# Optimization experiments

Measured on AMD Instinct MI355X. Metric: run time of the kernel, lower is better.

The kernel has to match this reference:

```python
import jax, jax.numpy as jnp
import numpy as np

T = 25
H1, H2, H3 = 16, 72, 32


def _lin_params(key, out_dim, in_dim):
    k1, k2 = jax.random.split(key)
    s = 1.0 / np.sqrt(in_dim)
    W = jax.random.uniform(k1, (out_dim, in_dim), jnp.float32, -s, s)
    b = jax.random.uniform(k2, (out_dim,), jnp.float32, -s, s)
    return W, b


def _lstm_params(key, in_dim, hid):
    k1, k2, k3, k4 = jax.random.split(key, 4)
    s = 1.0 / np.sqrt(hid)
    Wih = jax.random.uniform(k1, (4 * hid, in_dim), jnp.float32, -s, s)
    Whh = jax.random.uniform(k2, (4 * hid, hid), jnp.float32, -s, s)
    bih = jax.random.uniform(k3, (4 * hid,), jnp.float32, -s, s)
    bhh = jax.random.uniform(k4, (4 * hid,), jnp.float32, -s, s)
    return Wih, Whh, bih, bhh


def setup_inputs() -> dict:
    key = jax.random.key(0)
    ks = jax.random.split(key, 9)
    B = 131072
    x = jax.random.normal(ks[0], (B, T, 2), jnp.float32)
    y = jax.random.normal(ks[1], (B, T, 36), jnp.float32)
    Wih1, Whh1, bih1, bhh1 = _lstm_params(ks[2], 2, H1)
    Wih2, Whh2, bih2, bhh2 = _lstm_params(ks[3], H2, H2)
    Wih3, Whh3, bih3, bhh3 = _lstm_params(ks[4], H1 + H2, H3)
    W1, b1 = _lin_params(ks[5], 64, 36)
    W2, b2 = _lin_params(ks[6], H2, 64)
    W3, b3 = _lin_params(ks[7], 16, H3)
    W4, b4 = _lin_params(ks[8], 2, 16)
    return dict(x=x, y=y,
                Wih1=Wih1, Whh1=Whh1, bih1=bih1, bhh1=bhh1,
                Wih2=Wih2, Whh2=Whh2, bih2=bih2, bhh2=bhh2,
                Wih3=Wih3, Whh3=Whh3, bih3=bih3, bhh3=bhh3,
                W1=W1, b1=b1, W2=W2, b2=b2, W3=W3, b3=b3, W4=W4, b4=b4)


def _lstm_cell(xt, h, c, Wih, Whh, bih, bhh):
    # PyTorch LSTMCell gate order: i, f, g, o
    g = xt @ Wih.T + bih + h @ Whh.T + bhh
    i, f, gg, o = jnp.split(g, 4, axis=-1)
    c_new = jax.nn.sigmoid(f) * c + jax.nn.sigmoid(i) * jnp.tanh(gg)
    h_new = jax.nn.sigmoid(o) * jnp.tanh(c_new)
    return h_new, c_new


def _forward(x, y, Wih1, Whh1, bih1, bhh1, Wih2, Whh2, bih2, bhh2,
             Wih3, Whh3, bih3, bhh3, W1, b1, W2, b2, W3, b3, W4, b4):
    B = x.shape[0]
    init = (jnp.zeros((B, H1), jnp.float32), jnp.zeros((B, H1), jnp.float32),
            jnp.zeros((B, H2), jnp.float32), jnp.zeros((B, H2), jnp.float32),
            jnp.zeros((B, H3), jnp.float32), jnp.zeros((B, H3), jnp.float32))

    def step(carry, inp):
        h1, c1, h2, c2, h3, c3 = carry
        xt, yt = inp  # [B,2], [B,36]
        h1, c1 = _lstm_cell(xt, h1, c1, Wih1, Whh1, bih1, bhh1)
        l2 = jax.nn.relu(yt @ W1.T + b1) @ W2.T + b2
        h2, c2 = _lstm_cell(l2, h2, c2, Wih2, Whh2, bih2, bhh2)
        h = jnp.concatenate([h1, h2], axis=1)
        h3, c3 = _lstm_cell(h, h3, c3, Wih3, Whh3, bih3, bhh3)
        out = jax.nn.relu(h3 @ W3.T + b3) @ W4.T + b4  # [B,2]
        return (h1, c1, h2, c2, h3, c3), out

    xs = (jnp.swapaxes(x, 0, 1), jnp.swapaxes(y, 0, 1))  # [T,B,*]
    _, outs = jax.lax.scan(step, init, xs)  # [T,B,2]
    # torch.cat(outputs, dim=1) -> [B, T*2]
    return jnp.swapaxes(outs, 0, 1).reshape(B, T * 2)


def reference(x, y, Wih1, Whh1, bih1, bhh1, Wih2, Whh2, bih2, bhh2,
              Wih3, Whh3, bih3, bhh3, W1, b1, W2, b2, W3, b3, W4, b4):
    return _forward(x, y, Wih1, Whh1, bih1, bhh1, Wih2, Whh2, bih2, bhh2,
                    Wih3, Whh3, bih3, bhh3, W1, b1, W2, b2, W3, b3, W4, b4)
```

## Files before the change

### kernel.cpp

```cpp
#include <hip/hip_runtime.h>
#include <hip/hip_bf16.h>

#define THREADS 1024

typedef __hip_bfloat16 bf16;
typedef __attribute__((ext_vector_type(4))) float f32x4;
typedef __attribute__((ext_vector_type(16))) float f32x16;
typedef __attribute__((ext_vector_type(8))) short bf16x8;

#define MFMA32 __builtin_amdgcn_mfma_f32_32x32x16_bf16
#define Z16 f32x16{0.f,0.f,0.f,0.f,0.f,0.f,0.f,0.f,0.f,0.f,0.f,0.f,0.f,0.f,0.f,0.f}

#define O_A1  0
#define O_AY  4096
#define O_AT1 10240
#define O_A2  20480
#define O_AH3 40960
#define LDS_ELEMS 45056
#define LDS_BYTES (LDS_ELEMS * 2)

__device__ __forceinline__ int blk(int KC, int nt, int kc, int slot) {
    return ((nt * KC + kc) * 2 + slot) << 9;
}
__device__ __forceinline__ int eix(int col, int kl) {
    return ((col | ((kl >> 3) << 5)) << 3) + (kl & 7);
}

__device__ __forceinline__ float rcp_(float x) { return __builtin_amdgcn_rcpf(x); }

__device__ __forceinline__ float lstm_ew1(f32x4 acc, float& cst) {
    float ei = __expf(-acc[0]);
    float ef = __expf(-acc[1]);
    float eg = __expf(2.0f * fminf(acc[2], 40.0f));
    float eo = __expf(-acc[3]);
    float c = rcp_(1.0f + ef) * cst + (eg - 1.0f) * rcp_((1.0f + ei) * (eg + 1.0f));
    cst = c;
    float ec = __expf(2.0f * fminf(c, 40.0f));
    return (ec - 1.0f) * rcp_((1.0f + eo) * (ec + 1.0f));
}

__device__ __forceinline__ ushort bfu(float f) {
    union { bf16 b; ushort u; } v; v.b = __float2bfloat16(f); return v.u;
}

template <typename F>
__device__ __forceinline__ bf16x8 mk32(int lane, F val) {
    union { bf16x8 v; bf16 h[8]; } u;
#pragma unroll
    for (int j = 0; j < 8; ++j)
        u.h[j] = __float2bfloat16(val(((lane >> 5) << 3) + j));
    return u.v;
}

__global__ void __launch_bounds__(THREADS, 4)
lstm_fused(const float* __restrict__ x, const float* __restrict__ y,
           const float* __restrict__ Wih1, const float* __restrict__ Whh1,
           const float* __restrict__ bih1, const float* __restrict__ bhh1,
           const float* __restrict__ Wih2, const float* __restrict__ Whh2,
           const float* __restrict__ bih2, const float* __restrict__ bhh2,
           const float* __restrict__ Wih3, const float* __restrict__ Whh3,
           const float* __restrict__ bih3, const float* __restrict__ bhh3,
           const float* __restrict__ W1, const float* __restrict__ b1,
           const float* __restrict__ W2, const float* __restrict__ b2,
           const float* __restrict__ W3, const float* __restrict__ b3,
           const float* __restrict__ W4, const float* __restrict__ b4,
           float* __restrict__ out) {
    extern __shared__ char smem[];
    bf16* sb = (bf16*)smem;
    const int tid = threadIdx.x;
    const int wave = tid >> 6, lane = tid & 63;
    const int ln31 = lane & 31, hi = lane >> 5;
    const int b0 = blockIdx.x * 64;

    bf16x8 W[11];
#pragma unroll
    for (int i = 0; i < 11; ++i) W[i] = bf16x8{0, 0, 0, 0, 0, 0, 0, 0};

    if (wave < 9) {
        int n = 32 * wave + ln31;
        int r = (n & 3) * 72 + (n >> 2);
        float bias = bih2[r] + bhh2[r];
#pragma unroll
        for (int kc = 0; kc < 10; ++kc)
            W[kc] = mk32(lane, [&](int k) {
                int kg = kc * 16 + k;
                return kg < 72 ? Wih2[r * 72 + kg]
                     : (kg < 144 ? Whh2[r * 72 + (kg - 72)]
                     : (kg == 144 ? bias : 0.0f)); });
    } else if (wave < 13) {
        int n = 32 * (wave - 9) + ln31;
        int r = (n & 3) * 32 + (n >> 2);
        float bias = bih3[r] + bhh3[r];
        W[0] = mk32(lane, [&](int k) {
            return k < 2 ? 0.0f : Wih3[r * 88 + (k - 2)]; });
        W[1] = mk32(lane, [&](int k) {
            int kg = 16 + k;
            return kg < 18 ? Wih3[r * 88 + (kg - 2)] : (kg == 18 ? bias : 0.0f); });
#pragma unroll
        for (int i = 0; i < 5; ++i)
            W[2 + i] = mk32(lane, [&](int k) {
                int kg = 64 + i * 16 + k;
                return kg < 72 ? 0.0f : Wih3[r * 88 + 16 + (kg - 72)]; });
#pragma unroll
        for (int i = 0; i < 2; ++i)
            W[7 + i] = mk32(lane, [&](int k) { return Whh3[r * 32 + i * 16 + k]; });
        if (wave < 11) {
#pragma unroll
            for (int i = 0; i < 2; ++i)
                W[9 + i] = mk32(lane, [&](int k) {
                    return (ln31 < 16) ? W3[ln31 * 32 + i * 16 + k] : 0.0f; });
        }
    } else {
        if (wave < 15) {
            int n = 32 * (wave - 13) + ln31;
            int r = (n & 3) * 16 + (n >> 2);
            float bias = bih1[r] + bhh1[r];
            W[0] = mk32(lane, [&](int k) {
                return k < 2 ? Wih1[r * 2 + k] : Whh1[r * 16 + (k - 2)]; });
            W[1] = mk32(lane, [&](int k) {
                int kg = 16 + k;
                return kg < 18 ? Whh1[r * 16 + (kg - 2)] : (kg == 18 ? bias : 0.0f); });
        }
        {
            int n2 = 32 * (wave - 13) + ln31;
#pragma unroll
            for (int kc = 0; kc < 5; ++kc)
                W[2 + kc] = mk32(lane, [&](int k) {
                    int kg = kc * 16 + k;
                    if (n2 >= 72) return 0.0f;
                    return kg < 64 ? W2[n2 * 64 + kg] : (kg == 64 ? b2[n2] : 0.0f); });
        }
        if (wave >= 14) {
            int f = 32 * (wave - 14) + ln31;
#pragma unroll
            for (int kc = 0; kc < 3; ++kc)
                W[7 + kc] = mk32(lane, [&](int k) {
                    int kg = kc * 16 + k;
                    return kg < 36 ? W1[f * 36 + kg] : (kg == 36 ? b1[f] : 0.0f); });
        }
    }

    {
        int4* z = (int4*)sb;
        int4 zv = {0, 0, 0, 0};
        for (int i = tid; i < LDS_BYTES / 16; i += THREADS) z[i] = zv;
    }
    __syncthreads();
    for (int it = tid; it < 2 * 2304; it += THREADS) {
        int slot = it / 2304, r2 = it - slot * 2304;
        int m = r2 / 36, k = r2 - m * 36;
        sb[O_AY + blk(3, m >> 5, k >> 4, slot) + eix(m & 31, k & 15)] =
            __float2bfloat16(y[(size_t)(b0 + m) * 900 + slot * 36 + k]);
    }
    if (tid < 128) {
        int m = tid >> 1, k = tid & 1;
        sb[O_A1 + blk(2, m >> 5, 0, 0) + eix(m & 31, k)] =
            __float2bfloat16(x[(size_t)(b0 + m) * 50 + k]);
    }
    {
        const bf16 one = __float2bfloat16(1.0f);
        int i = tid & 127, col = i & 31, nt = (i >> 5) & 1, s = (i >> 6) & 1;
        if (tid < 128)       sb[O_A1 + blk(2, nt, 1, s) + eix(col, 2)] = one;
        else if (tid < 256)  sb[O_AY + blk(3, nt, 2, s) + eix(col, 4)] = one;
        else if (tid < 384)  sb[O_AT1 + blk(5, nt, 4, s) + eix(col, 0)] = one;
        else if (tid < 512)  sb[O_A2 + blk(10, nt, 9, s) + eix(col, 0)] = one;
    }
    __syncthreads();
    if (wave >= 14) {
#pragma unroll
        for (int s = 0; s < 2; ++s) {
#pragma unroll
            for (int nt = 0; nt < 2; ++nt) {
                f32x16 acc = Z16;
#pragma unroll
                for (int kc = 0; kc < 3; ++kc) {
                    bf16x8 a = *(const bf16x8*)(sb + O_AY + blk(3, nt, kc, s) + (lane << 3));
                    acc = MFMA32(W[7 + kc], a, acc, 0, 0, 0);
                }
#pragma unroll
                for (int qq = 0; qq < 4; ++qq) {
                    int f0 = 32 * (wave - 14) + 8 * qq + 4 * hi;
                    ushort4 pk;
                    pk.x = bfu(fmaxf(acc[4 * qq + 0], 0.f));
                    pk.y = bfu(fmaxf(acc[4 * qq + 1], 0.f));
                    pk.z = bfu(fmaxf(acc[4 * qq + 2], 0.f));
                    pk.w = bfu(fmaxf(acc[4 * qq + 3], 0.f));
                    *(ushort4*)(sb + O_AT1 + blk(5, nt, f0 >> 4, s ^ 1) + eix(ln31, f0 & 15)) = pk;
                }
            }
        }
    }
    __syncthreads();
    if (wave >= 13) {
#pragma unroll
        for (int nt = 0; nt < 2; ++nt) {
            f32x16 acc = Z16;
#pragma unroll
            for (int kc = 0; kc < 5; ++kc) {
                bf16x8 a = *(const bf16x8*)(sb + O_AT1 + blk(5, nt, kc, 1) + (lane << 3));
                acc = MFMA32(W[2 + kc], a, acc, 0, 0, 0);
            }
#pragma unroll
            for (int qq = 0; qq < 4; ++qq) {
                int n0 = 32 * (wave - 13) + 8 * qq + 4 * hi;
                if (n0 < 72) {
                    ushort4 pk;
                    pk.x = bfu(acc[4 * qq + 0]); pk.y = bfu(acc[4 * qq + 1]);
                    pk.z = bfu(acc[4 * qq + 2]); pk.w = bfu(acc[4 * qq + 3]);
                    *(ushort4*)(sb + O_A2 + blk(10, nt, n0 >> 4, 0) + eix(ln31, n0 & 15)) = pk;
                }
            }
        }
    } else if (wave == 11 || wave == 12) {
        const int half = wave - 11;
        const int m = 32 * half + (lane >> 1);
        const float* yp = y + (size_t)(b0 + m) * 900 + 2 * 36;
#pragma unroll
        for (int c = (lane & 1); c < 9; c += 2) {
            float4 v = *(const float4*)(yp + 4 * c);
            ushort4 pk;
            pk.x = bfu(v.x); pk.y = bfu(v.y); pk.z = bfu(v.z); pk.w = bfu(v.w);
            int k0 = 4 * c;
            *(ushort4*)(sb + O_AY + blk(3, half, k0 >> 4, 0) + eix(m & 31, k0 & 15)) = pk;
        }
    }
    float cS[2][4] = {};
    __syncthreads();

    for (int t = 0; t <= 25; ++t) {
        const int p = t & 1, q = p ^ 1;

        if (wave < 9) {
            if (t <= 24) {
#pragma unroll
                for (int nt = 0; nt < 2; ++nt) {
                    f32x16 acc = Z16;
#pragma unroll
                    for (int kc = 0; kc < 10; ++kc) {
                        bf16x8 a = *(const bf16x8*)(sb + O_A2 + blk(10, nt, kc, p) + (lane << 3));
                        acc = MFMA32(W[kc], a, acc, 0, 0, 0);
                    }
#pragma unroll
                    for (int qq = 0; qq < 4; ++qq) {
                        f32x4 g4 = {acc[4 * qq], acc[4 * qq + 1], acc[4 * qq + 2], acc[4 * qq + 3]};
                        float hv = lstm_ew1(g4, cS[nt][qq]);
                        int k = 72 + 8 * wave + 2 * qq + hi;
                        sb[O_A2 + blk(10, nt, k >> 4, q) + eix(ln31, k & 15)] = __float2bfloat16(hv);
                    }
                }
            }
        } else if (wave < 13) {
            if (t >= 1) {
                const int M3 = wave - 9;
#pragma unroll
                for (int nt = 0; nt < 2; ++nt) {
                    f32x16 acc = Z16;
                    {
                        bf16x8 a0 = *(const bf16x8*)(sb + O_A1 + blk(2, nt, 0, p) + (lane << 3));
                        acc = MFMA32(W[0], a0, acc, 0, 0, 0);
                        bf16x8 a1 = *(const bf16x8*)(sb + O_A1 + blk(2, nt, 1, p) + (lane << 3));
                        acc = MFMA32(W[1], a1, acc, 0, 0, 0);
                    }
#pragma unroll
                    for (int i = 0; i < 5; ++i) {
                        bf16x8 a = *(const bf16x8*)(sb + O_A2 + blk(10, nt, 4 + i, p) + (lane << 3));
                        acc = MFMA32(W[2 + i], a, acc, 0, 0, 0);
                    }
#pragma unroll
                    for (int i = 0; i < 2; ++i) {
                        bf16x8 a = *(const bf16x8*)(sb + O_AH3 + blk(2, nt, i, p) + (lane << 3));
                        acc = MFMA32(W[7 + i], a, acc, 0, 0, 0);
                    }
#pragma unroll
                    for (int qq = 0; qq < 4; ++qq) {
                        f32x4 g4 = {acc[4 * qq], acc[4 * qq + 1], acc[4 * qq + 2], acc[4 * qq + 3]};
                        float hv = lstm_ew1(g4, cS[nt][qq]);
                        int k = 8 * M3 + 2 * qq + hi;
                        sb[O_AH3 + blk(2, nt, k >> 4, q) + eix(ln31, k & 15)] = __float2bfloat16(hv);
                    }
                }
            }
            if (wave < 11) {
                if (t >= 2) {
                    const int ntw = wave - 9;
                    f32x16 acc = Z16;
#pragma unroll
                    for (int i = 0; i < 2; ++i) {
                        bf16x8 a = *(const bf16x8*)(sb + O_AH3 + blk(2, ntw, i, p) + (lane << 3));
                        acc = MFMA32(W[9 + i], a, acc, 0, 0, 0);
                    }
                    float s0 = 0.f, s1 = 0.f;
#pragma unroll
                    for (int qq = 0; qq < 2; ++qq) {
                        int r = 8 * qq + 4 * hi;
                        float4 b3v = *(const float4*)(b3 + r);
                        float4 w0v = *(const float4*)(W4 + r);
                        float4 w1v = *(const float4*)(W4 + 16 + r);
#pragma unroll
                        for (int s = 0; s < 4; ++s) {
                            float u = fmaxf(acc[4 * qq + s] + b3v[s], 0.f);
                            s0 = fmaf(u, w0v[s], s0);
                            s1 = fmaf(u, w1v[s], s1);
                        }
                    }
                    s0 += __shfl_xor(s0, 32); s1 += __shfl_xor(s1, 32);
                    if (lane < 32) {
                        float2 o; o.x = s0 + b4[0]; o.y = s1 + b4[1];
                        *(float2*)(out + (size_t)(b0 + 32 * ntw + ln31) * 50 + (t - 2) * 2) = o;
                    }
                }
            } else if (t <= 21) {
                const int half = wave - 11;
                const int m = 32 * half + (lane >> 1);
                const float* yp = y + (size_t)(b0 + m) * 900 + (t + 3) * 36;
#pragma unroll
                for (int c = (lane & 1); c < 9; c += 2) {
                    float4 v = *(const float4*)(yp + 4 * c);
                    ushort4 pk;
                    pk.x = bfu(v.x); pk.y = bfu(v.y); pk.z = bfu(v.z); pk.w = bfu(v.w);
                    int k0 = 4 * c;
                    *(ushort4*)(sb + O_AY + blk(3, half, k0 >> 4, q) + eix(m & 31, k0 & 15)) = pk;
                }
            }
        } else {
            if (t <= 24 && wave < 15) {
                const int M1 = wave - 13;
#pragma unroll
                for (int nt = 0; nt < 2; ++nt) {
                    f32x16 acc = Z16;
#pragma unroll
                    for (int i = 0; i < 2; ++i) {
                        bf16x8 a = *(const bf16x8*)(sb + O_A1 + blk(2, nt, i, p) + (lane << 3));
                        acc = MFMA32(W[i], a, acc, 0, 0, 0);
                    }
#pragma unroll
                    for (int qq = 0; qq < 4; ++qq) {
                        f32x4 g4 = {acc[4 * qq], acc[4 * qq + 1], acc[4 * qq + 2], acc[4 * qq + 3]};
                        float hv = lstm_ew1(g4, cS[nt][qq]);
                        int k = 2 + 8 * M1 + 2 * qq + hi;
                        sb[O_A1 + blk(2, nt, k >> 4, q) + eix(ln31, k & 15)] = __float2bfloat16(hv);
                    }
                }
            }
            if (t <= 23 && wave == 13) {
                const int nt = lane >> 5;
                float2 xv = *(const float2*)(x + (size_t)(b0 + lane) * 50 + (t + 1) * 2);
                union { uint u; ushort s[2]; } xu;
                xu.s[0] = bfu(xv.x); xu.s[1] = bfu(xv.y);
                *(uint*)(sb + O_A1 + blk(2, nt, 0, q) + (ln31 << 3)) = xu.u;
            }
            if (t <= 22 && wave >= 14) {
#pragma unroll
                for (int nt = 0; nt < 2; ++nt) {
                    f32x16 acc = Z16;
#pragma unroll
                    for (int kc = 0; kc < 3; ++kc) {
                        bf16x8 a = *(const bf16x8*)(sb + O_AY + blk(3, nt, kc, p) + (lane << 3));
                        acc = MFMA32(W[7 + kc], a, acc, 0, 0, 0);
                    }
#pragma unroll
                    for (int qq = 0; qq < 4; ++qq) {
                        int f0 = 32 * (wave - 14) + 8 * qq + 4 * hi;
                        ushort4 pk;
                        pk.x = bfu(fmaxf(acc[4 * qq + 0], 0.f));
                        pk.y = bfu(fmaxf(acc[4 * qq + 1], 0.f));
                        pk.z = bfu(fmaxf(acc[4 * qq + 2], 0.f));
                        pk.w = bfu(fmaxf(acc[4 * qq + 3], 0.f));
                        *(ushort4*)(sb + O_AT1 + blk(5, nt, f0 >> 4, q) + eix(ln31, f0 & 15)) = pk;
                    }
                }
            }
            if (t <= 23) {
#pragma unroll
                for (int nt = 0; nt < 2; ++nt) {
                    f32x16 acc = Z16;
#pragma unroll
                    for (int kc = 0; kc < 5; ++kc) {
                        bf16x8 a = *(const bf16x8*)(sb + O_AT1 + blk(5, nt, kc, p) + (lane << 3));
                        acc = MFMA32(W[2 + kc], a, acc, 0, 0, 0);
                    }
#pragma unroll
                    for (int qq = 0; qq < 4; ++qq) {
                        int n0 = 32 * (wave - 13) + 8 * qq + 4 * hi;
                        if (n0 < 72) {
                            ushort4 pk;
                            pk.x = bfu(acc[4 * qq + 0]); pk.y = bfu(acc[4 * qq + 1]);
                            pk.z = bfu(acc[4 * qq + 2]); pk.w = bfu(acc[4 * qq + 3]);
                            *(ushort4*)(sb + O_A2 + blk(10, nt, n0 >> 4, q) + eix(ln31, n0 & 15)) = pk;
                        }
                    }
                }
            }
        }
        __syncthreads();
    }

    if (wave == 9 || wave == 10) {
        const int ntw = wave - 9;
        f32x16 acc = Z16;
#pragma unroll
        for (int i = 0; i < 2; ++i) {
            bf16x8 a = *(const bf16x8*)(sb + O_AH3 + blk(2, ntw, i, 0) + (lane << 3));
            acc = MFMA32(W[9 + i], a, acc, 0, 0, 0);
        }
        float s0 = 0.f, s1 = 0.f;
#pragma unroll
        for (int qq = 0; qq < 2; ++qq) {
            int r = 8 * qq + 4 * hi;
            float4 b3v = *(const float4*)(b3 + r);
            float4 w0v = *(const float4*)(W4 + r);
            float4 w1v = *(const float4*)(W4 + 16 + r);
#pragma unroll
            for (int s = 0; s < 4; ++s) {
                float u = fmaxf(acc[4 * qq + s] + b3v[s], 0.f);
                s0 = fmaf(u, w0v[s], s0);
                s1 = fmaf(u, w1v[s], s1);
            }
        }
        s0 += __shfl_xor(s0, 32); s1 += __shfl_xor(s1, 32);
        if (lane < 32) {
            float2 o; o.x = s0 + b4[0]; o.y = s1 + b4[1];
            *(float2*)(out + (size_t)(b0 + 32 * ntw + ln31) * 50 + 24 * 2) = o;
        }
    }
}

extern "C" void kernel_launch(void* const* d_in, const int* in_sizes, int n_in,
                              void* d_out, int out_size, void* d_ws, size_t ws_size,
                              hipStream_t stream) {
    (void)in_sizes; (void)n_in; (void)d_ws; (void)ws_size; (void)out_size;
    hipFuncSetAttribute((const void*)lstm_fused,
                        hipFuncAttributeMaxDynamicSharedMemorySize, LDS_BYTES);
    lstm_fused<<<dim3(2048), dim3(THREADS), LDS_BYTES, stream>>>(
        (const float*)d_in[0], (const float*)d_in[1],
        (const float*)d_in[2], (const float*)d_in[3],
        (const float*)d_in[4], (const float*)d_in[5],
        (const float*)d_in[6], (const float*)d_in[7],
        (const float*)d_in[8], (const float*)d_in[9],
        (const float*)d_in[10], (const float*)d_in[11],
        (const float*)d_in[12], (const float*)d_in[13],
        (const float*)d_in[14], (const float*)d_in[15],
        (const float*)d_in[16], (const float*)d_in[17],
        (const float*)d_in[18], (const float*)d_in[19],
        (const float*)d_in[20], (const float*)d_in[21],
        (float*)d_out);
}
```

Before: 944.3 us.

## Fold exp2 scaling into LSTM weights and restructure per-step load/compute/store scheduling

Pre-scales gate weights and biases by -log2(e), or by 2*log2(e) for the g gate, so the gate nonlinearities use raw exp2 without a multiply. Restructures each timestep so all LDS operand loads for both tiles are issued up front and the MFMAs run back to back, with the elementwise work and LDS stores deferred to the end. Global loads for y and x are issued early to overlap latency. The output head now reuses the h3 operands already in registers instead of re-reading them from LDS. This raises register pressure, which could hurt occupancy or cause spills.

```diff
diff --git a/kernel.cpp b/kernel.cpp
--- a/kernel.cpp
+++ b/kernel.cpp
@@ -27,15 +27,22 @@
 }
 
 __device__ __forceinline__ float rcp_(float x) { return __builtin_amdgcn_rcpf(x); }
-
-__device__ __forceinline__ float lstm_ew1(f32x4 acc, float& cst) {
-    float ei = __expf(-acc[0]);
-    float ef = __expf(-acc[1]);
-    float eg = __expf(2.0f * fminf(acc[2], 40.0f));
-    float eo = __expf(-acc[3]);
+__device__ __forceinline__ float exp2_(float x) {
+#if __has_builtin(__builtin_amdgcn_exp2f)
+    return __builtin_amdgcn_exp2f(x);
+#else
+    return exp2f(x);
+#endif
+}
+
+__device__ __forceinline__ float lstm_ew1(f32x4 a, float& cst) {
+    float ei = exp2_(a[0]);
+    float ef = exp2_(a[1]);
+    float eg = exp2_(fminf(a[2], 115.0f));
+    float eo = exp2_(a[3]);
     float c = rcp_(1.0f + ef) * cst + (eg - 1.0f) * rcp_((1.0f + ei) * (eg + 1.0f));
     cst = c;
-    float ec = __expf(2.0f * fminf(c, 40.0f));
+    float ec = exp2_(fminf(c * 2.885390082f, 115.0f));
     return (ec - 1.0f) * rcp_((1.0f + eo) * (ec + 1.0f));
 }
 
@@ -80,30 +87,33 @@
         int n = 32 * wave + ln31;
         int r = (n & 3) * 72 + (n >> 2);
         float bias = bih2[r] + bhh2[r];
+        float sc = ((n & 3) == 2) ? 2.885390082f : -1.442695041f;
 #pragma unroll
         for (int kc = 0; kc < 10; ++kc)
             W[kc] = mk32(lane, [&](int k) {
                 int kg = kc * 16 + k;
-                return kg < 72 ? Wih2[r * 72 + kg]
-                     : (kg < 144 ? Whh2[r * 72 + (kg - 72)]
-                     : (kg == 144 ? bias : 0.0f)); });
+                float v = kg < 72 ? Wih2[r * 72 + kg]
+                       : (kg < 144 ? Whh2[r * 72 + (kg - 72)]
+                       : (kg == 144 ? bias : 0.0f));
+                return sc * v; });
     } else if (wave < 13) {
         int n = 32 * (wave - 9) + ln31;
         int r = (n & 3) * 32 + (n >> 2);
         float bias = bih3[r] + bhh3[r];
+        float sc = ((n & 3) == 2) ? 2.885390082f : -1.442695041f;
         W[0] = mk32(lane, [&](int k) {
-            return k < 2 ? 0.0f : Wih3[r * 88 + (k - 2)]; });
+            return sc * (k < 2 ? 0.0f : Wih3[r * 88 + (k - 2)]); });
         W[1] = mk32(lane, [&](int k) {
             int kg = 16 + k;
-            return kg < 18 ? Wih3[r * 88 + (kg - 2)] : (kg == 18 ? bias : 0.0f); });
+            return sc * (kg < 18 ? Wih3[r * 88 + (kg - 2)] : (kg == 18 ? bias : 0.0f)); });
 #pragma unroll
         for (int i = 0; i < 5; ++i)
             W[2 + i] = mk32(lane, [&](int k) {
                 int kg = 64 + i * 16 + k;
-                return kg < 72 ? 0.0f : Wih3[r * 88 + 16 + (kg - 72)]; });
+                return sc * (kg < 72 ? 0.0f : Wih3[r * 88 + 16 + (kg - 72)]); });
 #pragma unroll
         for (int i = 0; i < 2; ++i)
-            W[7 + i] = mk32(lane, [&](int k) { return Whh3[r * 32 + i * 16 + k]; });
+            W[7 + i] = mk32(lane, [&](int k) { return sc * Whh3[r * 32 + i * 16 + k]; });
         if (wave < 11) {
 #pragma unroll
             for (int i = 0; i < 2; ++i)
@@ -115,11 +125,12 @@
             int n = 32 * (wave - 13) + ln31;
             int r = (n & 3) * 16 + (n >> 2);
             float bias = bih1[r] + bhh1[r];
+            float sc = ((n & 3) == 2) ? 2.885390082f : -1.442695041f;
             W[0] = mk32(lane, [&](int k) {
-                return k < 2 ? Wih1[r * 2 + k] : Whh1[r * 16 + (k - 2)]; });
+                return sc * (k < 2 ? Wih1[r * 2 + k] : Whh1[r * 16 + (k - 2)]); });
             W[1] = mk32(lane, [&](int k) {
                 int kg = 16 + k;
-                return kg < 18 ? Whh1[r * 16 + (kg - 2)] : (kg == 18 ? bias : 0.0f); });
+                return sc * (kg < 18 ? Whh1[r * 16 + (kg - 2)] : (kg == 18 ? bias : 0.0f)); });
         }
         {
             int n2 = 32 * (wave - 13) + ln31;
@@ -232,164 +243,239 @@
 
         if (wave < 9) {
             if (t <= 24) {
-#pragma unroll
-                for (int nt = 0; nt < 2; ++nt) {
-                    f32x16 acc = Z16;
-#pragma unroll
-                    for (int kc = 0; kc < 10; ++kc) {
-                        bf16x8 a = *(const bf16x8*)(sb + O_A2 + blk(10, nt, kc, p) + (lane << 3));
-                        acc = MFMA32(W[kc], a, acc, 0, 0, 0);
+                bf16x8 al[10], bl[10];
+#pragma unroll
+                for (int kc = 0; kc < 10; ++kc)
+                    al[kc] = *(const bf16x8*)(sb + O_A2 + blk(10, 0, kc, p) + (lane << 3));
+                f32x16 acc0 = Z16;
+#pragma unroll
+                for (int kc = 0; kc < 10; ++kc) acc0 = MFMA32(W[kc], al[kc], acc0, 0, 0, 0);
+#pragma unroll
+                for (int kc = 0; kc < 10; ++kc)
+                    bl[kc] = *(const bf16x8*)(sb + O_A2 + blk(10, 1, kc, p) + (lane << 3));
+                f32x16 acc1 = Z16;
+#pragma unroll
+                for (int kc = 0; kc < 10; ++kc) acc1 = MFMA32(W[kc], bl[kc], acc1, 0, 0, 0);
+                ushort hv0[4], hv1[4];
+#pragma unroll
+                for (int qq = 0; qq < 4; ++qq) {
+                    f32x4 g4 = {acc0[4 * qq], acc0[4 * qq + 1], acc0[4 * qq + 2], acc0[4 * qq + 3]};
+                    hv0[qq] = bfu(lstm_ew1(g4, cS[0][qq]));
+                }
+#pragma unroll
+                for (int qq = 0; qq < 4; ++qq) {
+                    f32x4 g4 = {acc1[4 * qq], acc1[4 * qq + 1], acc1[4 * qq + 2], acc1[4 * qq + 3]};
+                    hv1[qq] = bfu(lstm_ew1(g4, cS[1][qq]));
+                }
+#pragma unroll
+                for (int qq = 0; qq < 4; ++qq) {
+                    int k = 72 + 8 * wave + 2 * qq + hi;
+                    *(ushort*)(sb + O_A2 + blk(10, 0, k >> 4, q) + eix(ln31, k & 15)) = hv0[qq];
+                    *(ushort*)(sb + O_A2 + blk(10, 1, k >> 4, q) + eix(ln31, k & 15)) = hv1[qq];
+                }
+            }
+        } else if (wave < 13) {
+            const bool ystage = (wave >= 11) && (t <= 21);
+            float4 yv[5];
+            if (ystage) {
+                const int m = 32 * (wave - 11) + (lane >> 1);
+                const float* yp = y + (size_t)(b0 + m) * 900 + (t + 3) * 36;
+#pragma unroll
+                for (int i = 0; i < 5; ++i) {
+                    int c = 2 * i + (lane & 1);
+                    if (c < 9) yv[i] = *(const float4*)(yp + 4 * c);
+                }
+            }
+            ushort hv0[4], hv1[4];
+            bf16x8 ahw0 = {}, ahw1 = {};
+            if (t >= 1) {
+                bf16x8 a[9], b[9];
+                a[0] = *(const bf16x8*)(sb + O_A1 + blk(2, 0, 0, p) + (lane << 3));
+                a[1] = *(const bf16x8*)(sb + O_A1 + blk(2, 0, 1, p) + (lane << 3));
+#pragma unroll
+                for (int i = 0; i < 5; ++i)
+                    a[2 + i] = *(const bf16x8*)(sb + O_A2 + blk(10, 0, 4 + i, p) + (lane << 3));
+                a[7] = *(const bf16x8*)(sb + O_AH3 + blk(2, 0, 0, p) + (lane << 3));
+                a[8] = *(const bf16x8*)(sb + O_AH3 + blk(2, 0, 1, p) + (lane << 3));
+                f32x16 acc0 = Z16;
+#pragma unroll
+                for (int i = 0; i < 9; ++i) acc0 = MFMA32(W[i], a[i], acc0, 0, 0, 0);
+                b[0] = *(const bf16x8*)(sb + O_A1 + blk(2, 1, 0, p) + (lane << 3));
+                b[1] = *(const bf16x8*)(sb + O_A1 + blk(2, 1, 1, p) + (lane << 3));
+#pragma unroll
+                for (int i = 0; i < 5; ++i)
+                    b[2 + i] = *(const bf16x8*)(sb + O_A2 + blk(10, 1, 4 + i, p) + (lane << 3));
+                b[7] = *(const bf16x8*)(sb + O_AH3 + blk(2, 1, 0, p) + (lane << 3));
+                b[8] = *(const bf16x8*)(sb + O_AH3 + blk(2, 1, 1, p) + (lane << 3));
+                f32x16 acc1 = Z16;
+#pragma unroll
+                for (int i = 0; i < 9; ++i) acc1 = MFMA32(W[i], b[i], acc1, 0, 0, 0);
+                if (wave == 9)  { ahw0 = a[7]; ahw1 = a[8]; }
+                if (wave == 10) { ahw0 = b[7]; ahw1 = b[8]; }
+#pragma unroll
+                for (int qq = 0; qq < 4; ++qq) {
+                    f32x4 g4 = {acc0[4 * qq], acc0[4 * qq + 1], acc0[4 * qq + 2], acc0[4 * qq + 3]};
+                    hv0[qq] = bfu(lstm_ew1(g4, cS[0][qq]));
+                }
+#pragma unroll
+                for (int qq = 0; qq < 4; ++qq) {
+                    f32x4 g4 = {acc1[4 * qq], acc1[4 * qq + 1], acc1[4 * qq + 2], acc1[4 * qq + 3]};
+                    hv1[qq] = bfu(lstm_ew1(g4, cS[1][qq]));
+                }
+            }
+            if (t >= 2 && wave < 11) {
+                const int ntw = wave - 9;
+                f32x16 acc = Z16;
+                acc = MFMA32(W[9], ahw0, acc, 0, 0, 0);
+                acc = MFMA32(W[10], ahw1, acc, 0, 0, 0);
+                float s0 = 0.f, s1 = 0.f;
+#pragma unroll
+                for (int qq = 0; qq < 2; ++qq) {
+                    int r = 8 * qq + 4 * hi;
+                    float4 b3v = *(const float4*)(b3 + r);
+                    float4 w0v = *(const float4*)(W4 + r);
+                    float4 w1v = *(const float4*)(W4 + 16 + r);
+#pragma unroll
+                    for (int s = 0; s < 4; ++s) {
+                        float u = fmaxf(acc[4 * qq + s] + b3v[s], 0.f);
+                        s0 = fmaf(u, w0v[s], s0);
+                        s1 = fmaf(u, w1v[s], s1);
                     }
-#pragma unroll
-                    for (int qq = 0; qq < 4; ++qq) {
-                        f32x4 g4 = {acc[4 * qq], acc[4 * qq + 1], acc[4 * qq + 2], acc[4 * qq + 3]};
-                        float hv = lstm_ew1(g4, cS[nt][qq]);
-                        int k = 72 + 8 * wave + 2 * qq + hi;
-                        sb[O_A2 + blk(10, nt, k >> 4, q) + eix(ln31, k & 15)] = __float2bfloat16(hv);
-                    }
-                }
-            }
-        } else if (wave < 13) {
+                }
+                s0 += __shfl_xor(s0, 32); s1 += __shfl_xor(s1, 32);
+                if (lane < 32) {
+                    float2 o; o.x = s0 + b4[0]; o.y = s1 + b4[1];
+                    *(float2*)(out + (size_t)(b0 + 32 * ntw + ln31) * 50 + (t - 2) * 2) = o;
+                }
+            }
             if (t >= 1) {
                 const int M3 = wave - 9;
 #pragma unroll
+                for (int qq = 0; qq < 4; ++qq) {
+                    int k = 8 * M3 + 2 * qq + hi;
+                    *(ushort*)(sb + O_AH3 + blk(2, 0, k >> 4, q) + eix(ln31, k & 15)) = hv0[qq];
+                    *(ushort*)(sb + O_AH3 + blk(2, 1, k >> 4, q) + eix(ln31, k & 15)) = hv1[qq];
+                }
+            }
+            if (ystage) {
+                const int m = 32 * (wave - 11) + (lane >> 1);
+#pragma unroll
+                for (int i = 0; i < 5; ++i) {
+                    int c = 2 * i + (lane & 1);
+                    if (c < 9) {
+                        ushort4 pk;
+                        pk.x = bfu(yv[i].x); pk.y = bfu(yv[i].y);
+                        pk.z = bfu(yv[i].z); pk.w = bfu(yv[i].w);
+                        int k0 = 4 * c;
+                        *(ushort4*)(sb + O_AY + blk(3, wave - 11, k0 >> 4, q) + eix(m & 31, k0 & 15)) = pk;
+                    }
+                }
+            }
+        } else {
+            float2 xv = {0.f, 0.f};
+            if (wave == 13 && t <= 23)
+                xv = *(const float2*)(x + (size_t)(b0 + lane) * 50 + (t + 1) * 2);
+            ushort hva[4], hvb[4];
+            if (t <= 24 && wave < 15) {
+                bf16x8 a0 = *(const bf16x8*)(sb + O_A1 + blk(2, 0, 0, p) + (lane << 3));
+                bf16x8 a1 = *(const bf16x8*)(sb + O_A1 + blk(2, 0, 1, p) + (lane << 3));
+                bf16x8 c0 = *(const bf16x8*)(sb + O_A1 + blk(2, 1, 0, p) + (lane << 3));
+                bf16x8 c1 = *(const bf16x8*)(sb + O_A1 + blk(2, 1, 1, p) + (lane << 3));
+                f32x16 acc0 = Z16, acc1 = Z16;
+                acc0 = MFMA32(W[0], a0, acc0, 0, 0, 0);
+                acc0 = MFMA32(W[1], a1, acc0, 0, 0, 0);
+                acc1 = MFMA32(W[0], c0, acc1, 0, 0, 0);
+                acc1 = MFMA32(W[1], c1, acc1, 0, 0, 0);
+#pragma unroll
+                for (int qq = 0; qq < 4; ++qq) {
+                    f32x4 g4 = {acc0[4 * qq], acc0[4 * qq + 1], acc0[4 * qq + 2], acc0[4 * qq + 3]};
+                    hva[qq] = bfu(lstm_ew1(g4, cS[0][qq]));
+                }
+#pragma unroll
+                for (int qq = 0; qq < 4; ++qq) {
+                    f32x4 g4 = {acc1[4 * qq], acc1[4 * qq + 1], acc1[4 * qq + 2], acc1[4 * qq + 3]};
+                    hvb[qq] = bfu(lstm_ew1(g4, cS[1][qq]));
+                }
+            }
+            ushort4 f1p[2][4];
+            if (t <= 22 && wave >= 14) {
+#pragma unroll
                 for (int nt = 0; nt < 2; ++nt) {
+                    bf16x8 a0 = *(const bf16x8*)(sb + O_AY + blk(3, nt, 0, p) + (lane << 3));
+                    bf16x8 a1 = *(const bf16x8*)(sb + O_AY + blk(3, nt, 1, p) + (lane << 3));
+                    bf16x8 a2 = *(const bf16x8*)(sb + O_AY + blk(3, nt, 2, p) + (lane << 3));
                     f32x16 acc = Z16;
-                    {
-                        bf16x8 a0 = *(const bf16x8*)(sb + O_A1 + blk(2, nt, 0, p) + (lane << 3));
-                        acc = MFMA32(W[0], a0, acc, 0, 0, 0);
-                        bf16x8 a1 = *(const bf16x8*)(sb + O_A1 + blk(2, nt, 1, p) + (lane << 3));
-                        acc = MFMA32(W[1], a1, acc, 0, 0, 0);
-                    }
-#pragma unroll
-                    for (int i = 0; i < 5; ++i) {
-                        bf16x8 a = *(const bf16x8*)(sb + O_A2 + blk(10, nt, 4 + i, p) + (lane << 3));
-                        acc = MFMA32(W[2 + i], a, acc, 0, 0, 0);
-                    }
-#pragma unroll
-                    for (int i = 0; i < 2; ++i) {
-                        bf16x8 a = *(const bf16x8*)(sb + O_AH3 + blk(2, nt, i, p) + (lane << 3));
-                        acc = MFMA32(W[7 + i], a, acc, 0, 0, 0);
-                    }
+                    acc = MFMA32(W[7], a0, acc, 0, 0, 0);
+                    acc = MFMA32(W[8], a1, acc, 0, 0, 0);
+                    acc = MFMA32(W[9], a2, acc, 0, 0, 0);
 #pragma unroll
                     for (int qq = 0; qq < 4; ++qq) {
-                        f32x4 g4 = {acc[4 * qq], acc[4 * qq + 1], acc[4 * qq + 2], acc[4 * qq + 3]};
-                        float hv = lstm_ew1(g4, cS[nt][qq]);
-                        int k = 8 * M3 + 2 * qq + hi;
-                        sb[O_AH3 + blk(2, nt, k >> 4, q) + eix(ln31, k & 15)] = __float2bfloat16(hv);
-                    }
-                }
-            }
-            if (wave < 11) {
-                if (t >= 2) {
-                    const int ntw = wave - 9;
-                    f32x16 acc = Z16;
-#pragma unroll
-                    for (int i = 0; i < 2; ++i) {
-                        bf16x8 a = *(const bf16x8*)(sb + O_AH3 + blk(2, ntw, i, p) + (lane << 3));
-                        acc = MFMA32(W[9 + i], a, acc, 0, 0, 0);
-                    }
-                    float s0 = 0.f, s1 = 0.f;
-#pragma unroll
-                    for (int qq = 0; qq < 2; ++qq) {
-                        int r = 8 * qq + 4 * hi;
-                        float4 b3v = *(const float4*)(b3 + r);
-                        float4 w0v = *(const float4*)(W4 + r);
-                        float4 w1v = *(const float4*)(W4 + 16 + r);
-#pragma unroll
-                        for (int s = 0; s < 4; ++s) {
-                            float u = fmaxf(acc[4 * qq + s] + b3v[s], 0.f);
-                            s0 = fmaf(u, w0v[s], s0);
-                            s1 = fmaf(u, w1v[s], s1);
-                        }
-                    }
-                    s0 += __shfl_xor(s0, 32); s1 += __shfl_xor(s1, 32);
-                    if (lane < 32) {
-                        float2 o; o.x = s0 + b4[0]; o.y = s1 + b4[1];
-                        *(float2*)(out + (size_t)(b0 + 32 * ntw + ln31) * 50 + (t - 2) * 2) = o;
-                    }
-                }
-            } else if (t <= 21) {
-                const int half = wave - 11;
-                const int m = 32 * half + (lane >> 1);
-                const float* yp = y + (size_t)(b0 + m) * 900 + (t + 3) * 36;
-#pragma unroll
-                for (int c = (lane & 1); c < 9; c += 2) {
-                    float4 v = *(const float4*)(yp + 4 * c);
-                    ushort4 pk;
-                    pk.x = bfu(v.x); pk.y = bfu(v.y); pk.z = bfu(v.z); pk.w = bfu(v.w);
-                    int k0 = 4 * c;
-                    *(ushort4*)(sb + O_AY + blk(3, half, k0 >> 4, q) + eix(m & 31, k0 & 15)) = pk;
-                }
-            }
-        } else {
-            if (t <= 24 && wave < 15) {
-                const int M1 = wave - 13;
-#pragma unroll
-                for (int nt = 0; nt < 2; ++nt) {
-                    f32x16 acc = Z16;
-#pragma unroll
-                    for (int i = 0; i < 2; ++i) {
-                        bf16x8 a = *(const bf16x8*)(sb + O_A1 + blk(2, nt, i, p) + (lane << 3));
-                        acc = MFMA32(W[i], a, acc, 0, 0, 0);
-                    }
-#pragma unroll
-                    for (int qq = 0; qq < 4; ++qq) {
-                        f32x4 g4 = {acc[4 * qq], acc[4 * qq + 1], acc[4 * qq + 2], acc[4 * qq + 3]};
-                        float hv = lstm_ew1(g4, cS[nt][qq]);
-                        int k = 2 + 8 * M1 + 2 * qq + hi;
-                        sb[O_A1 + blk(2, nt, k >> 4, q) + eix(ln31, k & 15)] = __float2bfloat16(hv);
-                    }
-                }
-            }
-            if (t <= 23 && wave == 13) {
-                const int nt = lane >> 5;
-                float2 xv = *(const float2*)(x + (size_t)(b0 + lane) * 50 + (t + 1) * 2);
-                union { uint u; ushort s[2]; } xu;
-                xu.s[0] = bfu(xv.x); xu.s[1] = bfu(xv.y);
-                *(uint*)(sb + O_A1 + blk(2, nt, 0, q) + (ln31 << 3)) = xu.u;
-            }
-            if (t <= 22 && wave >= 14) {
-#pragma unroll
-                for (int nt = 0; nt < 2; ++nt) {
-                    f32x16 acc = Z16;
-#pragma unroll
-                    for (int kc = 0; kc < 3; ++kc) {
-                        bf16x8 a = *(const bf16x8*)(sb + O_AY + blk(3, nt, kc, p) + (lane << 3));
-                        acc = MFMA32(W[7 + kc], a, acc, 0, 0, 0);
-                    }
-#pragma unroll
-                    for (int qq = 0; qq < 4; ++qq) {
-                        int f0 = 32 * (wave - 14) + 8 * qq + 4 * hi;
                         ushort4 pk;
                         pk.x = bfu(fmaxf(acc[4 * qq + 0], 0.f));
                         pk.y = bfu(fmaxf(acc[4 * qq + 1], 0.f));
                         pk.z = bfu(fmaxf(acc[4 * qq + 2], 0.f));
                         pk.w = bfu(fmaxf(acc[4 * qq + 3], 0.f));
-                        *(ushort4*)(sb + O_AT1 + blk(5, nt, f0 >> 4, q) + eix(ln31, f0 & 15)) = pk;
+                        f1p[nt][qq] = pk;
                     }
                 }
             }
+            ushort4 f2p[2][4];
             if (t <= 23) {
 #pragma unroll
                 for (int nt = 0; nt < 2; ++nt) {
+                    bf16x8 a0 = *(const bf16x8*)(sb + O_AT1 + blk(5, nt, 0, p) + (lane << 3));
+                    bf16x8 a1 = *(const bf16x8*)(sb + O_AT1 + blk(5, nt, 1, p) + (lane << 3));
+                    bf16x8 a2 = *(const bf16x8*)(sb + O_AT1 + blk(5, nt, 2, p) + (lane << 3));
+                    bf16x8 a3 = *(const bf16x8*)(sb + O_AT1 + blk(5, nt, 3, p) + (lane << 3));
+                    bf16x8 a4 = *(const bf16x8*)(sb + O_AT1 + blk(5, nt, 4, p) + (lane << 3));
                     f32x16 acc = Z16;
-#pragma unroll
-                    for (int kc = 0; kc < 5; ++kc) {
-                        bf16x8 a = *(const bf16x8*)(sb + O_AT1 + blk(5, nt, kc, p) + (lane << 3));
-                        acc = MFMA32(W[2 + kc], a, acc, 0, 0, 0);
+                    acc = MFMA32(W[2], a0, acc, 0, 0, 0);
+                    acc = MFMA32(W[3], a1, acc, 0, 0, 0);
+                    acc = MFMA32(W[4], a2, acc, 0, 0, 0);
+                    acc = MFMA32(W[5], a3, acc, 0, 0, 0);
+                    acc = MFMA32(W[6], a4, acc, 0, 0, 0);
+#pragma unroll
+                    for (int qq = 0; qq < 4; ++qq) {
+                        ushort4 pk;
+                        pk.x = bfu(acc[4 * qq + 0]); pk.y = bfu(acc[4 * qq + 1]);
+                        pk.z = bfu(acc[4 * qq + 2]); pk.w = bfu(acc[4 * qq + 3]);
+                        f2p[nt][qq] = pk;
                     }
+                }
+            }
+            if (t <= 24 && wave < 15) {
+                const int M1 = wave - 13;
+#pragma unroll
+                for (int qq = 0; qq < 4; ++qq) {
+                    int k = 2 + 8 * M1 + 2 * qq + hi;
+                    *(ushort*)(sb + O_A1 + blk(2, 0, k >> 4, q) + eix(ln31, k & 15)) = hva[qq];
+                    *(ushort*)(sb + O_A1 + blk(2, 1, k >> 4, q) + eix(ln31, k & 15)) = hvb[qq];
+                }
+            }
+            if (wave == 13 && t <= 23) {
+                const int nt = lane >> 5;
+                union { uint u; ushort s[2]; } xu;
+                xu.s[0] = bfu(xv.x); xu.s[1] = bfu(xv.y);
+                *(uint*)(sb + O_A1 + blk(2, nt, 0, q) + (ln31 << 3)) = xu.u;
+            }
+            if (t <= 22 && wave >= 14) {
+#pragma unroll
+                for (int nt = 0; nt < 2; ++nt)
+#pragma unroll
+                    for (int qq = 0; qq < 4; ++qq) {
+                        int f0 = 32 * (wave - 14) + 8 * qq + 4 * hi;
+                        *(ushort4*)(sb + O_AT1 + blk(5, nt, f0 >> 4, q) + eix(ln31, f0 & 15)) = f1p[nt][qq];
+                    }
+            }
+            if (t <= 23) {
+#pragma unroll
+                for (int nt = 0; nt < 2; ++nt)
 #pragma unroll
                     for (int qq = 0; qq < 4; ++qq) {
                         int n0 = 32 * (wave - 13) + 8 * qq + 4 * hi;
-                        if (n0 < 72) {
-                            ushort4 pk;
-                            pk.x = bfu(acc[4 * qq + 0]); pk.y = bfu(acc[4 * qq + 1]);
-                            pk.z = bfu(acc[4 * qq + 2]); pk.w = bfu(acc[4 * qq + 3]);
-                            *(ushort4*)(sb + O_A2 + blk(10, nt, n0 >> 4, q) + eix(ln31, n0 & 15)) = pk;
-                        }
+                        if (n0 < 72)
+                            *(ushort4*)(sb + O_A2 + blk(10, nt, n0 >> 4, q) + eix(ln31, n0 & 15)) = f2p[nt][qq];
                     }
-                }
             }
         }
         __syncthreads();
```

Measured after the change: 1.706 ms. 1.81x slower.
